# Performance work log

Measured on AMD Instinct MI355X. Metric: run time of the kernel, lower is better.

## Reference

```python
import jax, jax.numpy as jnp
import numpy as np
import math

TOKEN_DIM = 1024
NUM_HEADS = 16
HEAD_DIM = TOKEN_DIM // NUM_HEADS
T, B, N = 32, 32, 64


def setup_inputs() -> dict:
    key = jax.random.key(0)
    ks = jax.random.split(key, 9)
    query_vec = jax.random.normal(ks[0], (T, B, TOKEN_DIM), dtype=jnp.float32)
    tokens = jax.random.normal(ks[1], (T, B, N, TOKEN_DIM), dtype=jnp.float32)
    gate_logits = jax.random.normal(ks[2], (T, B, N), dtype=jnp.float32)
    scale = 1.0 / math.sqrt(TOKEN_DIM)
    Wq = jax.random.normal(ks[3], (TOKEN_DIM, TOKEN_DIM), dtype=jnp.float32) * scale
    Wk = jax.random.normal(ks[4], (TOKEN_DIM, TOKEN_DIM), dtype=jnp.float32) * scale
    Wv = jax.random.normal(ks[5], (TOKEN_DIM, TOKEN_DIM), dtype=jnp.float32) * scale
    bq = jnp.zeros((TOKEN_DIM,), dtype=jnp.float32)
    bk = jnp.zeros((TOKEN_DIM,), dtype=jnp.float32)
    bv = jnp.zeros((TOKEN_DIM,), dtype=jnp.float32)
    return {"query_vec": query_vec, "tokens": tokens, "gate_logits": gate_logits,
            "Wq": Wq, "bq": bq, "Wk": Wk, "bk": bk, "Wv": Wv, "bv": bv}


def reference(query_vec, tokens, gate_logits, Wq, bq, Wk, bk, Wv, bv):
    # QKV projections
    q = query_vec @ Wq + bq                      # [T,B,D]
    k = tokens @ Wk + bk                         # [T,B,N,D]
    v = tokens @ Wv + bv                         # [T,B,N,D]
    q = q.reshape(T, B, NUM_HEADS, HEAD_DIM)
    k = k.reshape(T, B, N, NUM_HEADS, HEAD_DIM)
    v = v.reshape(T, B, N, NUM_HEADS, HEAD_DIM)
    logits = jnp.einsum('tbhd,tbnhd->tbhn', q, k) / math.sqrt(HEAD_DIM)
    logits = logits + gate_logits[:, :, None, :]
    attn = jax.nn.softmax(logits, axis=-1)       # [T,B,H,N]
    attended = jnp.einsum('tbhn,tbnhd->tbhd', attn, v)
    attended = attended.reshape(T, B, TOKEN_DIM)
    mean_attn = attn.mean(axis=2)                # [T,B,N]
    return (attended, mean_attn, logits)
```

## Files before the change

### kernel.cpp

```cpp
#include <hip/hip_runtime.h>
#include <hip/hip_bf16.h>

typedef __attribute__((ext_vector_type(4))) float f32x4;
typedef __attribute__((ext_vector_type(8))) short bf16x8;
typedef unsigned int u32;
typedef unsigned short u16;

#define DEV static __device__ __forceinline__


DEV u16 f2bf(float x){
  union { float f; u32 u; } v; v.f = x;
  u32 r = v.u + 0x7FFFu + ((v.u >> 16) & 1u);
  return (u16)(r >> 16);
}
DEV float bf2f(u16 s){
  union { u32 u; float f; } v; v.u = ((u32)s) << 16;
  return v.f;
}

#define MFMA16(a,b,c) __builtin_amdgcn_mfma_f32_16x16x32_bf16((a),(b),(c),0,0,0)

#define SWZ(n) ((((n)&3)<<5) | ((((n)>>2)&1)<<4))

DEV void bar_lgkm(){
  __builtin_amdgcn_sched_barrier(0);
  asm volatile("s_waitcnt lgkmcnt(0)" ::: "memory");
  __builtin_amdgcn_s_barrier();
  __builtin_amdgcn_sched_barrier(0);
}
DEV void bar_full(){
  __builtin_amdgcn_sched_barrier(0);
  asm volatile("s_waitcnt vmcnt(0) lgkmcnt(0)" ::: "memory");
  __builtin_amdgcn_s_barrier();
  __builtin_amdgcn_sched_barrier(0);
}

DEV bf16x8 cvt8(f32x4 lo, f32x4 hi){
  union { u32 u[4]; bf16x8 v; } r;
  asm("v_cvt_pk_bf16_f32 %0, %1, %2" : "=v"(r.u[0]) : "v"(lo.x), "v"(lo.y));
  asm("v_cvt_pk_bf16_f32 %0, %1, %2" : "=v"(r.u[1]) : "v"(lo.z), "v"(lo.w));
  asm("v_cvt_pk_bf16_f32 %0, %1, %2" : "=v"(r.u[2]) : "v"(hi.x), "v"(hi.y));
  asm("v_cvt_pk_bf16_f32 %0, %1, %2" : "=v"(r.u[3]) : "v"(hi.z), "v"(hi.w));
  return r.v;
}

DEV void stage8(const float* __restrict__ tokens, int tbn, int tk0,
                char* smem, int bb, int w, int l){
  char* ldsb = smem + (size_t)bb*32768 + (size_t)w*8192;
  const char* gb = (const char*)tokens + (size_t)tbn*262144 + (size_t)tk0*4096;
  #pragma unroll
  for (int j = 0; j < 8; ++j){
    const int nloc  = w*2 + (j >> 2);
    const int inner = (((j & 3)*1024) + l*16) ^ SWZ(nloc);
    __builtin_amdgcn_global_load_lds(
        (const __attribute__((address_space(1))) u32*)(gb + (size_t)nloc*4096 + inner),
        (__attribute__((address_space(3))) u32*)(ldsb + j*1024),
        16, 0, 0);
  }
}

__global__ __launch_bounds__(256) void k_convert(
    const float* __restrict__ Wq, const float* __restrict__ Wk, const float* __restrict__ Wv,
    u16* __restrict__ WqT, u16* __restrict__ WkB, u16* __restrict__ WvT){
  __shared__ u16 tile[64][65];
  const int which = blockIdx.y;
  const float* src = which==0 ? Wq : (which==1 ? Wk : Wv);
  const int bi = (blockIdx.x >> 4) << 6;
  const int bj = (blockIdx.x & 15) << 6;
  const int t  = threadIdx.x;
  #pragma unroll
  for (int k2 = 0; k2 < 16; ++k2){
    int e = t + (k2 << 8);
    int r = e >> 6, c = e & 63;
    tile[r][c] = f2bf(src[(size_t)(bi + r)*1024 + bj + c]);
  }
  __syncthreads();
  if (which == 1){
    #pragma unroll
    for (int k2 = 0; k2 < 16; ++k2){
      int e = t + (k2 << 8); int r = e >> 6, c = e & 63;
      WkB[(size_t)(bi + r)*1024 + bj + c] = tile[r][c];
    }
  } else {
    u16* dst = which==0 ? WqT : WvT;
    #pragma unroll
    for (int k2 = 0; k2 < 16; ++k2){
      int e = t + (k2 << 8); int r = e >> 6, c = e & 63;
      dst[(size_t)(bj + r)*1024 + bi + c] = tile[c][r];
    }
  }
}

__global__ __launch_bounds__(256) void k_qproj(
    const float* __restrict__ qv, const u16* __restrict__ WqT, const float* __restrict__ bq,
    float* __restrict__ qf, u16* __restrict__ qb){
  const int l = threadIdx.x & 63, w = threadIdx.x >> 6;
  const int wm = w & 1, wn = w >> 1;
  const int g = l >> 4, li = l & 15;
  const int m_base = blockIdx.x*64 + wm*32;
  const int n_base = blockIdx.y*64 + wn*32;
  f32x4 acc[2][2];
  #pragma unroll
  for (int i=0;i<2;++i)
    #pragma unroll
    for (int j=0;j<2;++j) acc[i][j] = (f32x4)0.0f;

  #pragma unroll 4
  for (int kb = 0; kb < 32; ++kb){
    const int k0 = kb*32 + g*8;
    bf16x8 a[2], b[2];
    #pragma unroll
    for (int rt = 0; rt < 2; ++rt){
      const float* p = qv + (size_t)(m_base + rt*16 + li)*1024 + k0;
      f32x4 lo = *(const f32x4*)p;
      f32x4 hi = *(const f32x4*)(p+4);
      union { u16 s[8]; bf16x8 v; } u;
      u.s[0]=f2bf(lo.x); u.s[1]=f2bf(lo.y); u.s[2]=f2bf(lo.z); u.s[3]=f2bf(lo.w);
      u.s[4]=f2bf(hi.x); u.s[5]=f2bf(hi.y); u.s[6]=f2bf(hi.z); u.s[7]=f2bf(hi.w);
      a[rt] = u.v;
    }
    #pragma unroll
    for (int ct = 0; ct < 2; ++ct)
      b[ct] = *(const bf16x8*)(WqT + (size_t)(n_base + ct*16 + li)*1024 + k0);
    #pragma unroll
    for (int rt = 0; rt < 2; ++rt)
      #pragma unroll
      for (int ct = 0; ct < 2; ++ct)
        acc[rt][ct] = MFMA16(a[rt], b[ct], acc[rt][ct]);
  }
  #pragma unroll
  for (int rt=0;rt<2;++rt)
    #pragma unroll
    for (int ct=0;ct<2;++ct)
      #pragma unroll
      for (int r=0;r<4;++r){
        int m = m_base + rt*16 + g*4 + r;
        int n = n_base + ct*16 + li;
        float val = acc[rt][ct][r] + bq[n];
        qf[(size_t)m*1024 + n] = val;
        qb[(size_t)m*1024 + n] = f2bf(val);
      }
}

__global__ __launch_bounds__(256) void k_umat(
    const u16* __restrict__ qb, const u16* __restrict__ WkB, u16* __restrict__ U){
  __shared__ __align__(16) u16 stile[64][64];
  const int l = threadIdx.x & 63, w = threadIdx.x >> 6;
  const int wm = w & 1, wn = w >> 1, g = l >> 4, li = l & 15;
  const int tb0 = blockIdx.x*64, d0 = blockIdx.y*64, h = blockIdx.z;
  f32x4 acc[2][2];
  #pragma unroll
  for (int i=0;i<2;++i)
    #pragma unroll
    for (int j=0;j<2;++j) acc[i][j] = (f32x4)0.0f;

  #pragma unroll
  for (int kb = 0; kb < 2; ++kb){
    const int k0 = h*64 + kb*32 + g*8;
    bf16x8 a[2], b[2];
    #pragma unroll
    for (int rt=0;rt<2;++rt)
      a[rt] = *(const bf16x8*)(qb + (size_t)(tb0 + wm*32 + rt*16 + li)*1024 + k0);
    #pragma unroll
    for (int ct=0;ct<2;++ct)
      b[ct] = *(const bf16x8*)(WkB + (size_t)(d0 + wn*32 + ct*16 + li)*1024 + k0);
    #pragma unroll
    for (int rt=0;rt<2;++rt)
      #pragma unroll
      for (int ct=0;ct<2;++ct)
        acc[rt][ct] = MFMA16(a[rt], b[ct], acc[rt][ct]);
  }
  #pragma unroll
  for (int rt=0;rt<2;++rt)
    #pragma unroll
    for (int ct=0;ct<2;++ct)
      #pragma unroll
      for (int r=0;r<4;++r)
        stile[wm*32 + rt*16 + g*4 + r][wn*32 + ct*16 + li] = f2bf(acc[rt][ct][r]);
  __syncthreads();
  const int r = threadIdx.x >> 2, cg4 = threadIdx.x & 3;
  f32x4* dst = (f32x4*)(U + ((size_t)(tb0 + r)*16 + h)*1024 + d0 + cg4*16);
  const f32x4* s4 = (const f32x4*)(&stile[r][cg4*16]);
  dst[0] = s4[0]; dst[1] = s4[1];
}

#define K3_LDS 65536
__global__ __launch_bounds__(256, 2) void k_attn(
    const float* __restrict__ tokens, const float* __restrict__ gate,
    const u16* __restrict__ U, const float* __restrict__ qf, const float* __restrict__ bk,
    float* __restrict__ out_logits, float* __restrict__ out_mean, u16* __restrict__ ctx){
  extern __shared__ __align__(16) char smem[];
  __shared__ __align__(16) char sstat[9152];
  float* part_s   = (float*)(sstat);
  float* logits_s = (float*)(sstat + 4096);
  float* p_s      = (float*)(sstat + 8192);
  float* csum     = (float*)(sstat + 8704);
  float* gate_s   = (float*)(sstat + 8768);
  float* mzs      = (float*)(sstat + 9024);
  const int tb = blockIdx.x;
  const int tid = threadIdx.x;
  const int l = tid & 63, w = tid >> 6, g = l >> 4, li = l & 15;
  const int sh = tid >> 4, sj = tid & 15;

  bf16x8 a[8];
  const bf16x8* Ub = (const bf16x8*)(U + (size_t)tb*16384);
  #pragma unroll
  for (int i = 0; i < 8; ++i)
    a[i] = Ub[li*128 + (w*8 + i)*4 + g];

  if (tid < 64) gate_s[tid] = gate[(size_t)tb*64 + tid];
  {
    const float* qp = qf + (size_t)tb*1024 + sh*64 + sj*4;
    const float* bp = bk + sh*64 + sj*4;
    float part = qp[0]*bp[0] + qp[1]*bp[1] + qp[2]*bp[2] + qp[3]*bp[3];
    part += __shfl_xor(part, 1); part += __shfl_xor(part, 2);
    part += __shfl_xor(part, 4); part += __shfl_xor(part, 8);
    if (sj == 0) csum[sh] = part;
  }

  const int hl  = (l >> 3) & 3;
  const int hme = w*4 + hl;
  const int nme = l & 7;

  float m_run = -1e30f, z_run = 0.0f;
  f32x4 cacc[4][4];
  #pragma unroll
  for (int i=0;i<4;++i)
    #pragma unroll
    for (int j=0;j<4;++j) cacc[i][j] = (f32x4)0.0f;

  stage8(tokens, tb, 0, smem, 0, w, l);

  for (int r = 0; r < 8; ++r){
    const int n0 = r*8;
    char* bufc = smem + (size_t)(r & 1)*32768;

    bar_full();
    if (r + 1 < 8)
      stage8(tokens, tb, (r+1)*8, smem, (r+1) & 1, w, l);

    {
      const int row = li & 7;
      const int sw  = SWZ(row);
      f32x4 acc = (f32x4)0.0f;
      #pragma unroll
      for (int i = 0; i < 8; ++i){
        const int p0b = (w*8 + i)*128 + g*32;
        f32x4 lo = *(const f32x4*)(bufc + row*4096 + ((p0b     ) ^ sw));
        f32x4 hi = *(const f32x4*)(bufc + row*4096 + ((p0b + 16) ^ sw));
        acc = MFMA16(a[i], cvt8(lo, hi), acc);
      }
      *(f32x4*)(part_s + (size_t)(w*64 + l)*4) = acc;
    }
    bar_lgkm();

    float rsc;
    {
      const int base = w*64 + nme*4 + (hme & 3);
      float lv = part_s[base] + part_s[256 + base] + part_s[512 + base] + part_s[768 + base];
      lv = (lv + csum[hme])*0.125f + gate_s[n0 + nme];
      float cm = lv;
      cm = fmaxf(cm, __shfl_xor(cm, 1));
      cm = fmaxf(cm, __shfl_xor(cm, 2));
      cm = fmaxf(cm, __shfl_xor(cm, 4));
      float m_new = fmaxf(m_run, cm);
      rsc = __expf(m_run - m_new);
      float p0 = __expf(lv - m_new);
      float zs = p0;
      zs += __shfl_xor(zs, 1); zs += __shfl_xor(zs, 2); zs += __shfl_xor(zs, 4);
      z_run = z_run * rsc + zs;
      m_run = m_new;
      if (l < 32){
        p_s[nme*16 + hme] = p0;
        logits_s[hme*64 + n0 + nme] = lv;
      }
    }

    {
      float rr4[4];
      #pragma unroll
      for (int hh = 0; hh < 4; ++hh) rr4[hh] = __shfl(rsc, hh*8);
      #pragma unroll
      for (int dq = 0; dq < 4; ++dq)
        #pragma unroll
        for (int hh = 0; hh < 4; ++hh) cacc[dq][hh] *= rr4[hh];
      #pragma unroll
      for (int nl = 0; nl < 8; ++nl){
        const f32x4 p = *(const f32x4*)(p_s + nl*16 + w*4);
        const int swn = SWZ(nl);
        #pragma unroll
        for (int dq = 0; dq < 4; ++dq){
          const f32x4 t = *(const f32x4*)(bufc + (size_t)nl*4096 + ((dq*1024 + l*16) ^ swn));
          #pragma unroll
          for (int hh = 0; hh < 4; ++hh)
            cacc[dq][hh] += t * p[hh];
        }
      }
    }
  }

  if (l < 32 && (l & 7) == 0){
    mzs[hme*2]     = m_run;
    mzs[hme*2 + 1] = 1.0f / z_run;
  }
  bar_lgkm();

  {
    f32x4 v = *(const f32x4*)(logits_s + tid*4);
    *(f32x4*)(out_logits + (size_t)tb*1024 + tid*4) = v;
  }
  if (tid < 64){
    float s = 0.0f;
    #pragma unroll
    for (int h = 0; h < 16; ++h)
      s += __expf(logits_s[h*64 + tid] - mzs[h*2]) * mzs[h*2 + 1];
    out_mean[(size_t)tb*64 + tid] = s * 0.0625f;
  }
  #pragma unroll
  for (int hh = 0; hh < 4; ++hh){
    const int h = w*4 + hh;
    const float zinv = mzs[h*2 + 1];
    #pragma unroll
    for (int dq = 0; dq < 4; ++dq){
      f32x4 v = cacc[dq][hh];
      uint2 pk;
      pk.x = (u32)f2bf(v.x * zinv) | ((u32)f2bf(v.y * zinv) << 16);
      pk.y = (u32)f2bf(v.z * zinv) | ((u32)f2bf(v.w * zinv) << 16);
      *(uint2*)(ctx + ((size_t)tb*16 + h)*1024 + dq*256 + l*4) = pk;
    }
  }
}

__global__ __launch_bounds__(256) void k_attended(
    const u16* __restrict__ ctx, const u16* __restrict__ WvT, const float* __restrict__ bv,
    float* __restrict__ out_att){
  const int l = threadIdx.x & 63, w = threadIdx.x >> 6;
  const int wm = w & 1, wn = w >> 1, g = l >> 4, li = l & 15;
  const int tb0 = blockIdx.x*64, h = blockIdx.y;
  f32x4 acc[2][2];
  #pragma unroll
  for (int i=0;i<2;++i)
    #pragma unroll
    for (int j=0;j<2;++j) acc[i][j] = (f32x4)0.0f;

  #pragma unroll 4
  for (int kb = 0; kb < 32; ++kb){
    const int k0 = kb*32 + g*8;
    bf16x8 a[2], b[2];
    #pragma unroll
    for (int rt=0;rt<2;++rt)
      a[rt] = *(const bf16x8*)(ctx + ((size_t)(tb0 + wm*32 + rt*16 + li)*16 + h)*1024 + k0);
    #pragma unroll
    for (int ct=0;ct<2;++ct)
      b[ct] = *(const bf16x8*)(WvT + (size_t)(h*64 + wn*32 + ct*16 + li)*1024 + k0);
    #pragma unroll
    for (int rt=0;rt<2;++rt)
      #pragma unroll
      for (int ct=0;ct<2;++ct)
        acc[rt][ct] = MFMA16(a[rt], b[ct], acc[rt][ct]);
  }
  #pragma unroll
  for (int rt=0;rt<2;++rt)
    #pragma unroll
    for (int ct=0;ct<2;++ct)
      #pragma unroll
      for (int r=0;r<4;++r){
        int m = tb0 + wm*32 + rt*16 + g*4 + r;
        int dout = h*64 + wn*32 + ct*16 + li;
        out_att[(size_t)m*1024 + dout] = acc[rt][ct][r] + bv[dout];
      }
}

extern "C" void kernel_launch(void* const* d_in, const int* in_sizes, int n_in,
                              void* d_out, int out_size, void* d_ws, size_t ws_size,
                              hipStream_t stream){
  const float* qv     = (const float*)d_in[0];
  const float* tokens = (const float*)d_in[1];
  const float* gate   = (const float*)d_in[2];
  const float* Wq     = (const float*)d_in[3];
  const float* bq     = (const float*)d_in[4];
  const float* Wk     = (const float*)d_in[5];
  const float* bk     = (const float*)d_in[6];
  const float* Wv     = (const float*)d_in[7];
  const float* bv     = (const float*)d_in[8];

  char* ws = (char*)d_ws;
  u16*   WqT = (u16*)(ws);
  u16*   WkB = (u16*)(ws + (2u<<20));
  u16*   WvT = (u16*)(ws + (4u<<20));
  float* qf  = (float*)(ws + (6u<<20));
  u16*   qb  = (u16*)(ws + (10u<<20));
  u16*   U   = (u16*)(ws + (12u<<20));
  u16*   ctxb= (u16*)(ws + (44u<<20));

  float* out_att    = (float*)d_out;
  float* out_mean   = out_att + 1048576;
  float* out_logits = out_att + 1114112;

  (void)hipFuncSetAttribute((const void*)k_attn,
                            hipFuncAttributeMaxDynamicSharedMemorySize, K3_LDS);
  k_convert <<<dim3(256, 3),    256, 0,      stream>>>(Wq, Wk, Wv, WqT, WkB, WvT);
  k_qproj   <<<dim3(16, 16),    256, 0,      stream>>>(qv, WqT, bq, qf, qb);
  k_umat    <<<dim3(16, 16, 16),256, 0,      stream>>>(qb, WkB, U);
  k_attn    <<<dim3(1024),      256, K3_LDS, stream>>>(tokens, gate, U, qf, bk,
                                                       out_logits, out_mean, ctxb);
  k_attended<<<dim3(16, 16),    256, 0,      stream>>>(ctxb, WvT, bv, out_att);
}
```

Baseline: 159.9 us.

## Compute full logits per wave redundantly to drop cross-wave LDS reduction

Each wave now computes the full 1024-long logit dot product for all 16 heads itself, with 32 MFMAs over the whole K dimension, instead of each wave covering a quarter of K and reducing partials through LDS. Softmax statistics for four heads per lane are kept in registers, and probabilities are broadcast with shuffles rather than through a shared p_s buffer, which removes a barrier and LDS traffic per round. The cost is four times the MFMA and LDS-read work for logits, and 32 bf16x8 registers per thread for the U fragments, which raises register pressure and may limit occupancy. Dynamic LDS is also replaced by a static allocation.

```diff
diff --git a/kernel.cpp b/kernel.cpp
--- a/kernel.cpp
+++ b/kernel.cpp
@@ -185,29 +185,26 @@
   dst[0] = s4[0]; dst[1] = s4[1];
 }
 
-#define K3_LDS 65536
 __global__ __launch_bounds__(256, 2) void k_attn(
     const float* __restrict__ tokens, const float* __restrict__ gate,
     const u16* __restrict__ U, const float* __restrict__ qf, const float* __restrict__ bk,
     float* __restrict__ out_logits, float* __restrict__ out_mean, u16* __restrict__ ctx){
-  extern __shared__ __align__(16) char smem[];
-  __shared__ __align__(16) char sstat[9152];
-  float* part_s   = (float*)(sstat);
-  float* logits_s = (float*)(sstat + 4096);
-  float* p_s      = (float*)(sstat + 8192);
-  float* csum     = (float*)(sstat + 8704);
-  float* gate_s   = (float*)(sstat + 8768);
-  float* mzs      = (float*)(sstat + 9024);
+  __shared__ __align__(16) char smem[65536];
+  __shared__ __align__(16) char sstat[4608];
+  float* logits_s = (float*)(sstat);
+  float* csum     = (float*)(sstat + 4096);
+  float* gate_s   = (float*)(sstat + 4160);
+  float* mzs      = (float*)(sstat + 4416);
   const int tb = blockIdx.x;
   const int tid = threadIdx.x;
   const int l = tid & 63, w = tid >> 6, g = l >> 4, li = l & 15;
   const int sh = tid >> 4, sj = tid & 15;
 
-  bf16x8 a[8];
+  bf16x8 a[32];
   const bf16x8* Ub = (const bf16x8*)(U + (size_t)tb*16384);
   #pragma unroll
-  for (int i = 0; i < 8; ++i)
-    a[i] = Ub[li*128 + (w*8 + i)*4 + g];
+  for (int i = 0; i < 32; ++i)
+    a[i] = Ub[li*128 + i*4 + g];
 
   if (tid < 64) gate_s[tid] = gate[(size_t)tb*64 + tid];
   {
@@ -218,19 +215,20 @@
     part += __shfl_xor(part, 4); part += __shfl_xor(part, 8);
     if (sj == 0) csum[sh] = part;
   }
-
-  const int hl  = (l >> 3) & 3;
-  const int hme = w*4 + hl;
-  const int nme = l & 7;
-
-  float m_run = -1e30f, z_run = 0.0f;
+  stage8(tokens, tb, 0, smem, 0, w, l);
+  bar_lgkm();
+  float csr[4];
+  #pragma unroll
+  for (int r4 = 0; r4 < 4; ++r4) csr[r4] = csum[g*4 + r4];
+
+  float m_run[4], z_run[4];
+  #pragma unroll
+  for (int r4 = 0; r4 < 4; ++r4){ m_run[r4] = -1e30f; z_run[r4] = 0.0f; }
   f32x4 cacc[4][4];
   #pragma unroll
   for (int i=0;i<4;++i)
     #pragma unroll
     for (int j=0;j<4;++j) cacc[i][j] = (f32x4)0.0f;
-
-  stage8(tokens, tb, 0, smem, 0, w, l);
 
   for (int r = 0; r < 8; ++r){
     const int n0 = r*8;
@@ -240,69 +238,72 @@
     if (r + 1 < 8)
       stage8(tokens, tb, (r+1)*8, smem, (r+1) & 1, w, l);
 
+    f32x4 acc = (f32x4)0.0f;
     {
       const int row = li & 7;
       const int sw  = SWZ(row);
-      f32x4 acc = (f32x4)0.0f;
-      #pragma unroll
-      for (int i = 0; i < 8; ++i){
-        const int p0b = (w*8 + i)*128 + g*32;
+      #pragma unroll
+      for (int i = 0; i < 32; ++i){
+        const int p0b = i*128 + g*32;
         f32x4 lo = *(const f32x4*)(bufc + row*4096 + ((p0b     ) ^ sw));
         f32x4 hi = *(const f32x4*)(bufc + row*4096 + ((p0b + 16) ^ sw));
         acc = MFMA16(a[i], cvt8(lo, hi), acc);
       }
-      *(f32x4*)(part_s + (size_t)(w*64 + l)*4) = acc;
-    }
-    bar_lgkm();
-
-    float rsc;
+    }
+
+    float pp[4], rsc[4];
     {
-      const int base = w*64 + nme*4 + (hme & 3);
-      float lv = part_s[base] + part_s[256 + base] + part_s[512 + base] + part_s[768 + base];
-      lv = (lv + csum[hme])*0.125f + gate_s[n0 + nme];
-      float cm = lv;
-      cm = fmaxf(cm, __shfl_xor(cm, 1));
-      cm = fmaxf(cm, __shfl_xor(cm, 2));
-      cm = fmaxf(cm, __shfl_xor(cm, 4));
-      float m_new = fmaxf(m_run, cm);
-      rsc = __expf(m_run - m_new);
-      float p0 = __expf(lv - m_new);
-      float zs = p0;
-      zs += __shfl_xor(zs, 1); zs += __shfl_xor(zs, 2); zs += __shfl_xor(zs, 4);
-      z_run = z_run * rsc + zs;
-      m_run = m_new;
-      if (l < 32){
-        p_s[nme*16 + hme] = p0;
-        logits_s[hme*64 + n0 + nme] = lv;
+      const float gv = gate_s[n0 + (li & 7)];
+      #pragma unroll
+      for (int r4 = 0; r4 < 4; ++r4){
+        float lv = (acc[r4] + csr[r4])*0.125f + gv;
+        float cm = lv;
+        cm = fmaxf(cm, __shfl_xor(cm, 1));
+        cm = fmaxf(cm, __shfl_xor(cm, 2));
+        cm = fmaxf(cm, __shfl_xor(cm, 4));
+        float m_new = fmaxf(m_run[r4], cm);
+        rsc[r4] = __expf(m_run[r4] - m_new);
+        pp[r4]  = __expf(lv - m_new);
+        float zs = pp[r4];
+        zs += __shfl_xor(zs, 1); zs += __shfl_xor(zs, 2); zs += __shfl_xor(zs, 4);
+        z_run[r4] = z_run[r4]*rsc[r4] + zs;
+        m_run[r4] = m_new;
+        if (w == 0 && li < 8)
+          logits_s[(g*4 + r4)*64 + n0 + li] = lv;
       }
     }
 
     {
       float rr4[4];
       #pragma unroll
-      for (int hh = 0; hh < 4; ++hh) rr4[hh] = __shfl(rsc, hh*8);
+      for (int hh = 0; hh < 4; ++hh) rr4[hh] = __shfl(rsc[hh], w*16);
       #pragma unroll
       for (int dq = 0; dq < 4; ++dq)
         #pragma unroll
         for (int hh = 0; hh < 4; ++hh) cacc[dq][hh] *= rr4[hh];
       #pragma unroll
       for (int nl = 0; nl < 8; ++nl){
-        const f32x4 p = *(const f32x4*)(p_s + nl*16 + w*4);
+        float pv[4];
+        #pragma unroll
+        for (int hh = 0; hh < 4; ++hh) pv[hh] = __shfl(pp[hh], w*16 + nl);
         const int swn = SWZ(nl);
         #pragma unroll
         for (int dq = 0; dq < 4; ++dq){
           const f32x4 t = *(const f32x4*)(bufc + (size_t)nl*4096 + ((dq*1024 + l*16) ^ swn));
           #pragma unroll
           for (int hh = 0; hh < 4; ++hh)
-            cacc[dq][hh] += t * p[hh];
+            cacc[dq][hh] += t * pv[hh];
         }
       }
     }
   }
 
-  if (l < 32 && (l & 7) == 0){
-    mzs[hme*2]     = m_run;
-    mzs[hme*2 + 1] = 1.0f / z_run;
+  if (w == 0 && li == 0){
+    #pragma unroll
+    for (int r4 = 0; r4 < 4; ++r4){
+      mzs[(g*4 + r4)*2]     = m_run[r4];
+      mzs[(g*4 + r4)*2 + 1] = 1.0f / z_run[r4];
+    }
   }
   bar_lgkm();
 
@@ -398,12 +399,10 @@
   float* out_mean   = out_att + 1048576;
   float* out_logits = out_att + 1114112;
 
-  (void)hipFuncSetAttribute((const void*)k_attn,
-                            hipFuncAttributeMaxDynamicSharedMemorySize, K3_LDS);
-  k_convert <<<dim3(256, 3),    256, 0,      stream>>>(Wq, Wk, Wv, WqT, WkB, WvT);
-  k_qproj   <<<dim3(16, 16),    256, 0,      stream>>>(qv, WqT, bq, qf, qb);
-  k_umat    <<<dim3(16, 16, 16),256, 0,      stream>>>(qb, WkB, U);
-  k_attn    <<<dim3(1024),      256, K3_LDS, stream>>>(tokens, gate, U, qf, bk,
-                                                       out_logits, out_mean, ctxb);
-  k_attended<<<dim3(16, 16),    256, 0,      stream>>>(ctxb, WvT, bv, out_att);
-}
+  k_convert <<<dim3(256, 3),    256, 0, stream>>>(Wq, Wk, Wv, WqT, WkB, WvT);
+  k_qproj   <<<dim3(16, 16),    256, 0, stream>>>(qv, WqT, bq, qf, qb);
+  k_umat    <<<dim3(16, 16, 16),256, 0, stream>>>(qb, WkB, U);
+  k_attn    <<<dim3(1024),      256, 0, stream>>>(tokens, gate, U, qf, bk,
+                                                  out_logits, out_mean, ctxb);
+  k_attended<<<dim3(16, 16),    256, 0, stream>>>(ctxb, WvT, bv, out_att);
+}
```

New measurement: 326.9 us. 104% more time.

## Convert staged tokens to bf16 once in LDS and raise attention occupancy

Applied to the files above, without the earlier changes.

The attention kernel now loads each fp32 token chunk into a single 32KB staging buffer and converts it once into a swizzled 16KB bf16 buffer. Both the logit MFMA and the value accumulation then read from that buffer, which replaces the 64KB double-buffered fp32 LDS and the repeated per-use conversions. Less LDS allows launch bounds of 3 blocks per CU. Logits are written straight to global memory and re-read to compute the mean-attention reduction with shuffles. The cost is an extra conversion pass with barriers between stages, weaker overlap of the loads with compute, and bf16 rounding of the values in the context accumulation.

```diff
diff --git a/kernel.cpp b/kernel.cpp
--- a/kernel.cpp
+++ b/kernel.cpp
@@ -21,7 +21,7 @@
 
 #define MFMA16(a,b,c) __builtin_amdgcn_mfma_f32_16x16x32_bf16((a),(b),(c),0,0,0)
 
-#define SWZ(n) ((((n)&3)<<5) | ((((n)>>2)&1)<<4))
+#define SWZB(n) ((((n)&3)<<5) | (((n)&4)<<2))
 
 DEV void bar_lgkm(){
   __builtin_amdgcn_sched_barrier(0);
@@ -36,23 +36,14 @@
   __builtin_amdgcn_sched_barrier(0);
 }
 
-DEV bf16x8 cvt8(f32x4 lo, f32x4 hi){
-  union { u32 u[4]; bf16x8 v; } r;
-  asm("v_cvt_pk_bf16_f32 %0, %1, %2" : "=v"(r.u[0]) : "v"(lo.x), "v"(lo.y));
-  asm("v_cvt_pk_bf16_f32 %0, %1, %2" : "=v"(r.u[1]) : "v"(lo.z), "v"(lo.w));
-  asm("v_cvt_pk_bf16_f32 %0, %1, %2" : "=v"(r.u[2]) : "v"(hi.x), "v"(hi.y));
-  asm("v_cvt_pk_bf16_f32 %0, %1, %2" : "=v"(r.u[3]) : "v"(hi.z), "v"(hi.w));
-  return r.v;
-}
-
-DEV void stage8(const float* __restrict__ tokens, int tbn, int tk0,
-                char* smem, int bb, int w, int l){
-  char* ldsb = smem + (size_t)bb*32768 + (size_t)w*8192;
+DEV void stage8L(const float* __restrict__ tokens, int tbn, int tk0,
+                 char* L, int w, int l){
+  char* ldsb = L + (size_t)w*8192;
   const char* gb = (const char*)tokens + (size_t)tbn*262144 + (size_t)tk0*4096;
   #pragma unroll
   for (int j = 0; j < 8; ++j){
     const int nloc  = w*2 + (j >> 2);
-    const int inner = (((j & 3)*1024) + l*16) ^ SWZ(nloc);
+    const int inner = (j & 3)*1024 + l*16;
     __builtin_amdgcn_global_load_lds(
         (const __attribute__((address_space(1))) u32*)(gb + (size_t)nloc*4096 + inner),
         (__attribute__((address_space(3))) u32*)(ldsb + j*1024),
@@ -185,19 +176,19 @@
   dst[0] = s4[0]; dst[1] = s4[1];
 }
 
-#define K3_LDS 65536
-__global__ __launch_bounds__(256, 2) void k_attn(
+__global__ __launch_bounds__(256, 3) void k_attn(
     const float* __restrict__ tokens, const float* __restrict__ gate,
     const u16* __restrict__ U, const float* __restrict__ qf, const float* __restrict__ bk,
     float* __restrict__ out_logits, float* __restrict__ out_mean, u16* __restrict__ ctx){
-  extern __shared__ __align__(16) char smem[];
-  __shared__ __align__(16) char sstat[9152];
-  float* part_s   = (float*)(sstat);
-  float* logits_s = (float*)(sstat + 4096);
-  float* p_s      = (float*)(sstat + 8192);
-  float* csum     = (float*)(sstat + 8704);
-  float* gate_s   = (float*)(sstat + 8768);
-  float* mzs      = (float*)(sstat + 9024);
+  __shared__ __align__(16) char Lz[32768];
+  __shared__ __align__(16) char Yb[16384];
+  __shared__ __align__(16) char sstat[4032];
+  float* part_s = (float*)(sstat);
+  float* p_s    = (float*)(sstat + 2048);
+  float* csum   = (float*)(sstat + 2560);
+  float* gate_s = (float*)(sstat + 2624);
+  float* mzs    = (float*)(sstat + 2880);
+  float* meanp  = (float*)(sstat + 3008);
   const int tb = blockIdx.x;
   const int tid = threadIdx.x;
   const int l = tid & 63, w = tid >> 6, g = l >> 4, li = l & 15;
@@ -219,8 +210,7 @@
     if (sj == 0) csum[sh] = part;
   }
 
-  const int hl  = (l >> 3) & 3;
-  const int hme = w*4 + hl;
+  const int hme = w*4 + ((l >> 3) & 3);
   const int nme = l & 7;
 
   float m_run = -1e30f, z_run = 0.0f;
@@ -230,35 +220,44 @@
     #pragma unroll
     for (int j=0;j<4;++j) cacc[i][j] = (f32x4)0.0f;
 
-  stage8(tokens, tb, 0, smem, 0, w, l);
+  stage8L(tokens, tb, 0, Lz, w, l);
+  bar_full();
+  #pragma unroll
+  for (int j = 0; j < 8; ++j){
+    f32x4 v = *(const f32x4*)(Lz + j*4096 + tid*16);
+    uint2 pk;
+    asm("v_cvt_pk_bf16_f32 %0, %1, %2" : "=v"(pk.x) : "v"(v.x), "v"(v.y));
+    asm("v_cvt_pk_bf16_f32 %0, %1, %2" : "=v"(pk.y) : "v"(v.z), "v"(v.w));
+    *(uint2*)(Yb + j*2048 + ((tid*8) ^ SWZB(j))) = pk;
+  }
+  bar_lgkm();
+  stage8L(tokens, tb, 8, Lz, w, l);
 
   for (int r = 0; r < 8; ++r){
     const int n0 = r*8;
-    char* bufc = smem + (size_t)(r & 1)*32768;
-
-    bar_full();
-    if (r + 1 < 8)
-      stage8(tokens, tb, (r+1)*8, smem, (r+1) & 1, w, l);
 
     {
-      const int row = li & 7;
-      const int sw  = SWZ(row);
+      const int tok = li & 7;
+      const int sw  = SWZB(tok);
       f32x4 acc = (f32x4)0.0f;
       #pragma unroll
       for (int i = 0; i < 8; ++i){
-        const int p0b = (w*8 + i)*128 + g*32;
-        f32x4 lo = *(const f32x4*)(bufc + row*4096 + ((p0b     ) ^ sw));
-        f32x4 hi = *(const f32x4*)(bufc + row*4096 + ((p0b + 16) ^ sw));
-        acc = MFMA16(a[i], cvt8(lo, hi), acc);
-      }
-      *(f32x4*)(part_s + (size_t)(w*64 + l)*4) = acc;
+        const int off = w*512 + i*64 + g*16;
+        bf16x8 b = *(const bf16x8*)(Yb + tok*2048 + (off ^ sw));
+        acc = MFMA16(a[i], b, acc);
+      }
+      if (li < 8){
+        #pragma unroll
+        for (int r4 = 0; r4 < 4; ++r4)
+          part_s[w*128 + (g*4 + r4)*8 + li] = acc[r4];
+      }
     }
     bar_lgkm();
 
     float rsc;
     {
-      const int base = w*64 + nme*4 + (hme & 3);
-      float lv = part_s[base] + part_s[256 + base] + part_s[512 + base] + part_s[768 + base];
+      const int bi = hme*8 + nme;
+      float lv = part_s[bi] + part_s[128 + bi] + part_s[256 + bi] + part_s[384 + bi];
       lv = (lv + csum[hme])*0.125f + gate_s[n0 + nme];
       float cm = lv;
       cm = fmaxf(cm, __shfl_xor(cm, 1));
@@ -269,11 +268,11 @@
       float p0 = __expf(lv - m_new);
       float zs = p0;
       zs += __shfl_xor(zs, 1); zs += __shfl_xor(zs, 2); zs += __shfl_xor(zs, 4);
-      z_run = z_run * rsc + zs;
+      z_run = z_run*rsc + zs;
       m_run = m_new;
       if (l < 32){
         p_s[nme*16 + hme] = p0;
-        logits_s[hme*64 + n0 + nme] = lv;
+        out_logits[(size_t)tb*1024 + hme*64 + n0 + nme] = lv;
       }
     }
 
@@ -288,35 +287,65 @@
       #pragma unroll
       for (int nl = 0; nl < 8; ++nl){
         const f32x4 p = *(const f32x4*)(p_s + nl*16 + w*4);
-        const int swn = SWZ(nl);
+        const int sw = SWZB(nl);
         #pragma unroll
         for (int dq = 0; dq < 4; ++dq){
-          const f32x4 t = *(const f32x4*)(bufc + (size_t)nl*4096 + ((dq*1024 + l*16) ^ swn));
+          uint2 t2 = *(const uint2*)(Yb + nl*2048 + ((dq*512 + l*8) ^ sw));
+          float f0 = bf2f((u16)(t2.x & 0xFFFFu));
+          float f1 = bf2f((u16)(t2.x >> 16));
+          float f2 = bf2f((u16)(t2.y & 0xFFFFu));
+          float f3 = bf2f((u16)(t2.y >> 16));
           #pragma unroll
-          for (int hh = 0; hh < 4; ++hh)
-            cacc[dq][hh] += t * p[hh];
+          for (int hh = 0; hh < 4; ++hh){
+            float av = p[hh];
+            cacc[dq][hh].x += av*f0; cacc[dq][hh].y += av*f1;
+            cacc[dq][hh].z += av*f2; cacc[dq][hh].w += av*f3;
+          }
         }
       }
     }
-  }
-
-  if (l < 32 && (l & 7) == 0){
+
+    bar_full();
+    if (r + 1 < 8){
+      #pragma unroll
+      for (int j = 0; j < 8; ++j){
+        f32x4 v = *(const f32x4*)(Lz + j*4096 + tid*16);
+        uint2 pk;
+        asm("v_cvt_pk_bf16_f32 %0, %1, %2" : "=v"(pk.x) : "v"(v.x), "v"(v.y));
+        asm("v_cvt_pk_bf16_f32 %0, %1, %2" : "=v"(pk.y) : "v"(v.z), "v"(v.w));
+        *(uint2*)(Yb + j*2048 + ((tid*8) ^ SWZB(j))) = pk;
+      }
+      bar_lgkm();
+      if (r + 2 < 8)
+        stage8L(tokens, tb, (r + 2)*8, Lz, w, l);
+    }
+  }
+
+  if (l < 32 && nme == 0){
     mzs[hme*2]     = m_run;
     mzs[hme*2 + 1] = 1.0f / z_run;
   }
+  bar_full();
+
+  {
+    f32x4 lg = *(const f32x4*)(out_logits + (size_t)tb*1024 + tid*4);
+    const int h = tid >> 4;
+    const float mh = mzs[h*2], zi = mzs[h*2 + 1];
+    f32x4 c;
+    c.x = __expf(lg.x - mh)*zi; c.y = __expf(lg.y - mh)*zi;
+    c.z = __expf(lg.z - mh)*zi; c.w = __expf(lg.w - mh)*zi;
+    c.x += __shfl_xor(c.x, 16); c.y += __shfl_xor(c.y, 16);
+    c.z += __shfl_xor(c.z, 16); c.w += __shfl_xor(c.w, 16);
+    c.x += __shfl_xor(c.x, 32); c.y += __shfl_xor(c.y, 32);
+    c.z += __shfl_xor(c.z, 32); c.w += __shfl_xor(c.w, 32);
+    if (l < 16) *(f32x4*)(meanp + w*64 + l*4) = c;
+  }
   bar_lgkm();
-
-  {
-    f32x4 v = *(const f32x4*)(logits_s + tid*4);
-    *(f32x4*)(out_logits + (size_t)tb*1024 + tid*4) = v;
-  }
   if (tid < 64){
-    float s = 0.0f;
-    #pragma unroll
-    for (int h = 0; h < 16; ++h)
-      s += __expf(logits_s[h*64 + tid] - mzs[h*2]) * mzs[h*2 + 1];
+    float s = meanp[tid] + meanp[64 + tid] + meanp[128 + tid] + meanp[192 + tid];
     out_mean[(size_t)tb*64 + tid] = s * 0.0625f;
   }
+
   #pragma unroll
   for (int hh = 0; hh < 4; ++hh){
     const int h = w*4 + hh;
@@ -398,12 +427,10 @@
   float* out_mean   = out_att + 1048576;
   float* out_logits = out_att + 1114112;
 
-  (void)hipFuncSetAttribute((const void*)k_attn,
-                            hipFuncAttributeMaxDynamicSharedMemorySize, K3_LDS);
-  k_convert <<<dim3(256, 3),    256, 0,      stream>>>(Wq, Wk, Wv, WqT, WkB, WvT);
-  k_qproj   <<<dim3(16, 16),    256, 0,      stream>>>(qv, WqT, bq, qf, qb);
-  k_umat    <<<dim3(16, 16, 16),256, 0,      stream>>>(qb, WkB, U);
-  k_attn    <<<dim3(1024),      256, K3_LDS, stream>>>(tokens, gate, U, qf, bk,
-                                                       out_logits, out_mean, ctxb);
-  k_attended<<<dim3(16, 16),    256, 0,      stream>>>(ctxb, WvT, bv, out_att);
-}
+  k_convert <<<dim3(256, 3),    256, 0, stream>>>(Wq, Wk, Wv, WqT, WkB, WvT);
+  k_qproj   <<<dim3(16, 16),    256, 0, stream>>>(qv, WqT, bq, qf, qb);
+  k_umat    <<<dim3(16, 16, 16),256, 0, stream>>>(qb, WkB, U);
+  k_attn    <<<dim3(1024),      256, 0, stream>>>(tokens, gate, U, qf, bk,
+                                                  out_logits, out_mean, ctxb);
+  k_attended<<<dim3(16, 16),    256, 0, stream>>>(ctxb, WvT, bv, out_att);
+}
```

After: 396.5 us. +148.0%, slower.
